# Performance work log

Hardware: AMD Instinct MI355X
Metric: run time of the kernel (lower is better)

## Reference

```python
import jax, jax.numpy as jnp
import numpy as np

B, S, D, UNITS = 8, 2048, 1024, 1024

def setup_inputs() -> dict:
    key = jax.random.key(0)
    k1, k2, k3, k4 = jax.random.split(key, 4)
    scale = 1.0 / np.sqrt(D)
    return {
        "inputs": jax.random.normal(k1, (B, S, D), dtype=jnp.float32),
        "Wq": jax.random.normal(k2, (D, UNITS), dtype=jnp.float32) * scale,
        "Wk": jax.random.normal(k3, (D, UNITS), dtype=jnp.float32) * scale,
        "Wv": jax.random.normal(k4, (D, UNITS), dtype=jnp.float32) * scale,
    }

def reference(inputs, Wq, Wk, Wv):
    # QKV projections (bias-free Dense): [B,S,D] @ [D,U] -> [B,S,U]
    q = jnp.einsum("bsd,du->bsu", inputs, Wq)
    k = jnp.einsum("bsd,du->bsu", inputs, Wk)
    v = jnp.einsum("bsd,du->bsu", inputs, Wv)
    # scaled dot-product scores [B,S,S]
    scores = jnp.einsum("bqu,bku->bqk", q, k) / jnp.sqrt(jnp.float32(UNITS))
    attn = jax.nn.softmax(scores, axis=-1)
    # weighted sum of values [B,S,U]
    return jnp.einsum("bqk,bku->bqu", attn, v)
```

## Files before the change

kernel.cpp:

```cpp
#include <hip/hip_runtime.h>


#define BM 128
#define BN 128
#define BK 64

typedef _Float16 half8  __attribute__((ext_vector_type(8)));
typedef _Float16 half4v __attribute__((ext_vector_type(4)));
typedef _Float16 half2v __attribute__((ext_vector_type(2)));
typedef float    floatx4 __attribute__((ext_vector_type(4)));

__device__ __forceinline__ void stage_async(const _Float16* __restrict__ src, int ld,
                                            _Float16* __restrict__ dst, int wave, int lane) {
#pragma unroll
    for (int i = 0; i < 4; ++i) {
        int chunk = i * 4 + wave;
        int L = chunk * 64 + lane;
        int row = L >> 3, c8 = L & 7;
        int cg = c8 ^ (row & 7);
        __builtin_amdgcn_global_load_lds(
            (const __attribute__((address_space(1))) unsigned int*)(src + (size_t)row * ld + cg * 8),
            (__attribute__((address_space(3))) unsigned int*)(dst + chunk * 512),
            16, 0, 0);
    }
}

__device__ __forceinline__ void mfma_accum(const _Float16* __restrict__ As,
                                           const _Float16* __restrict__ Bs,
                                           int wm, int wn, int l15, int q4,
                                           floatx4 acc[4][4]) {
#pragma unroll
    for (int kk = 0; kk < 2; ++kk) {
        half8 a[4], b[4];
#pragma unroll
        for (int i = 0; i < 4; ++i) {
            int row = wm * 64 + i * 16 + l15;
            int cg = (kk * 4 + q4) ^ (row & 7);
            a[i] = *(const half8*)(As + row * 64 + cg * 8);
        }
#pragma unroll
        for (int j = 0; j < 4; ++j) {
            int row = wn * 64 + j * 16 + l15;
            int cg = (kk * 4 + q4) ^ (row & 7);
            b[j] = *(const half8*)(Bs + row * 64 + cg * 8);
        }
#pragma unroll
        for (int i = 0; i < 4; ++i)
#pragma unroll
            for (int j = 0; j < 4; ++j)
                acc[i][j] = __builtin_amdgcn_mfma_f32_16x16x32_f16(a[i], b[j], acc[i][j], 0, 0, 0);
    }
}

__device__ __forceinline__ float sum8h(half8 a) {
    union { half8 v; half2v h2[4]; } u; u.v = a;
    half2v s0 = u.h2[0] + u.h2[1];
    half2v s1 = u.h2[2] + u.h2[3];
    half2v s  = s0 + s1;
    return (float)s[0] + (float)s[1];
}

__global__ void cast_x(const float* __restrict__ X, _Float16* __restrict__ Xh) {
    size_t i = ((size_t)blockIdx.x * 256 + threadIdx.x) * 8;
    float4 v0 = *(const float4*)(X + i);
    float4 v1 = *(const float4*)(X + i + 4);
    half8 hh;
    hh[0] = (_Float16)v0.x; hh[1] = (_Float16)v0.y; hh[2] = (_Float16)v0.z; hh[3] = (_Float16)v0.w;
    hh[4] = (_Float16)v1.x; hh[5] = (_Float16)v1.y; hh[6] = (_Float16)v1.z; hh[7] = (_Float16)v1.w;
    *(half8*)(Xh + i) = hh;
}

__global__ void prep_weights(const float* __restrict__ Wq, const float* __restrict__ Wk,
                             const float* __restrict__ Wv, _Float16* __restrict__ WbT) {
    int g = blockIdx.z;
    const float* W = (g == 0) ? Wq : (g == 1) ? Wk : Wv;
    __shared__ float tile[32][33];
    int u0 = blockIdx.x * 32, d0 = blockIdx.y * 32;
    int tx = threadIdx.x & 31, ty = threadIdx.x >> 5;
#pragma unroll
    for (int i = 0; i < 32; i += 8)
        tile[ty + i][tx] = W[(size_t)(d0 + ty + i) * 1024 + (u0 + tx)];
    __syncthreads();
#pragma unroll
    for (int i = 0; i < 32; i += 8)
        WbT[(size_t)g * 1024 * 1024 + (size_t)(u0 + ty + i) * 1024 + (d0 + tx)] =
            (_Float16)tile[tx][ty + i];
}

__global__ void qkv_gemm(const _Float16* __restrict__ Xh, const _Float16* __restrict__ WbT,
                         _Float16* __restrict__ Qh, _Float16* __restrict__ Kh,
                         _Float16* __restrict__ Vt) {
    __shared__ __align__(16) _Float16 As[BM * BK];
    __shared__ __align__(16) _Float16 Bs[BN * BK];
    int t = threadIdx.x;
    int lane = t & 63, wave = t >> 6;
    int wm = wave >> 1, wn = wave & 1;
    int l15 = lane & 15, q4 = lane >> 4;
    int m0 = blockIdx.y * BM, n0 = blockIdx.x * BN;
    floatx4 acc[4][4] = {};
    for (int kt = 0; kt < 1024; kt += BK) {
        __syncthreads();
        stage_async(Xh + (size_t)m0 * 1024 + kt, 1024, As, wave, lane);
        stage_async(WbT + (size_t)n0 * 1024 + kt, 1024, Bs, wave, lane);
        __syncthreads();
        mfma_accum(As, Bs, wm, wn, l15, q4, acc);
    }
    int which = blockIdx.x >> 3;
    int u0 = (blockIdx.x & 7) * BN;
    int b = m0 >> 11;
    int sbase = (m0 & 2047) + wm * 64;
    if (which < 2) {
        _Float16* dst = which ? Kh : Qh;
        _Float16* db = dst + (size_t)b * 2048 * 1024;
#pragma unroll
        for (int i = 0; i < 4; ++i)
#pragma unroll
            for (int j = 0; j < 4; ++j)
#pragma unroll
                for (int r = 0; r < 4; ++r) {
                    int s = sbase + i * 16 + q4 * 4 + r;
                    int u = u0 + wn * 64 + j * 16 + l15;
                    db[(size_t)s * 1024 + u] = (_Float16)acc[i][j][r];
                }
    } else {
        _Float16* vb = Vt + (size_t)b * 1024 * 2048;
#pragma unroll
        for (int i = 0; i < 4; ++i)
#pragma unroll
            for (int j = 0; j < 4; ++j) {
                int s = sbase + i * 16 + q4 * 4;
                int u = u0 + wn * 64 + j * 16 + l15;
                half4v pk;
#pragma unroll
                for (int r = 0; r < 4; ++r) pk[r] = (_Float16)acc[i][j][r];
                *(half4v*)(vb + (size_t)u * 2048 + s) = pk;
            }
    }
}

__global__ void scores_gemm(const _Float16* __restrict__ Qh, const _Float16* __restrict__ Kh,
                            _Float16* __restrict__ P) {
    __shared__ __align__(16) _Float16 As[BM * BK];
    __shared__ __align__(16) _Float16 Bs[BN * BK];
    int t = threadIdx.x;
    int lane = t & 63, wave = t >> 6;
    int wm = wave >> 1, wn = wave & 1;
    int l15 = lane & 15, q4 = lane >> 4;
    int m0 = blockIdx.y * BM, n0 = blockIdx.x * BN;
    int batch = blockIdx.z;
    const _Float16* A = Qh + (size_t)batch * 2048 * 1024;
    const _Float16* B = Kh + (size_t)batch * 2048 * 1024;
    floatx4 acc[4][4] = {};
    for (int kt = 0; kt < 1024; kt += BK) {
        __syncthreads();
        stage_async(A + (size_t)m0 * 1024 + kt, 1024, As, wave, lane);
        stage_async(B + (size_t)n0 * 1024 + kt, 1024, Bs, wave, lane);
        __syncthreads();
        mfma_accum(As, Bs, wm, wn, l15, q4, acc);
    }
    _Float16* Pb = P + (size_t)batch * 2048 * 2048;
#pragma unroll
    for (int i = 0; i < 4; ++i)
#pragma unroll
        for (int j = 0; j < 4; ++j)
#pragma unroll
            for (int r = 0; r < 4; ++r) {
                int m = m0 + wm * 64 + i * 16 + q4 * 4 + r;
                int n = n0 + wn * 64 + j * 16 + l15;
                Pb[(size_t)m * 2048 + n] = (_Float16)__expf(acc[i][j][r] * 0.03125f);
            }
}

__global__ void pv_gemm(const _Float16* __restrict__ P, const _Float16* __restrict__ Vt,
                        float* __restrict__ out) {
    __shared__ __align__(16) _Float16 As[BM * BK];
    __shared__ __align__(16) _Float16 Bs[BN * BK];
    int t = threadIdx.x;
    int lane = t & 63, wave = t >> 6;
    int wm = wave >> 1, wn = wave & 1;
    int l15 = lane & 15, q4 = lane >> 4;
    int m0 = blockIdx.y * BM, n0 = blockIdx.x * BN;
    int batch = blockIdx.z;
    const _Float16* A = P + (size_t)batch * 2048 * 2048;
    const _Float16* B = Vt + (size_t)batch * 1024 * 2048;
    floatx4 acc[4][4] = {};
    float rsum[4] = {0.f, 0.f, 0.f, 0.f};
    for (int kt = 0; kt < 2048; kt += BK) {
        __syncthreads();
        stage_async(A + (size_t)m0 * 2048 + kt, 2048, As, wave, lane);
        stage_async(B + (size_t)n0 * 2048 + kt, 2048, Bs, wave, lane);
        __syncthreads();
#pragma unroll
        for (int kk = 0; kk < 2; ++kk) {
            half8 a[4], b[4];
#pragma unroll
            for (int i = 0; i < 4; ++i) {
                int row = wm * 64 + i * 16 + l15;
                int cg = (kk * 4 + q4) ^ (row & 7);
                a[i] = *(const half8*)(As + row * 64 + cg * 8);
                rsum[i] += sum8h(a[i]);
            }
#pragma unroll
            for (int j = 0; j < 4; ++j) {
                int row = wn * 64 + j * 16 + l15;
                int cg = (kk * 4 + q4) ^ (row & 7);
                b[j] = *(const half8*)(Bs + row * 64 + cg * 8);
            }
#pragma unroll
            for (int i = 0; i < 4; ++i)
#pragma unroll
                for (int j = 0; j < 4; ++j)
                    acc[i][j] = __builtin_amdgcn_mfma_f32_16x16x32_f16(a[i], b[j], acc[i][j], 0, 0, 0);
        }
    }
    float rsumf[4];
#pragma unroll
    for (int i = 0; i < 4; ++i) {
        float v = rsum[i] + __shfl_xor(rsum[i], 16);
        rsumf[i] = v + __shfl_xor(v, 32);
    }
    float* ob = out + (size_t)batch * 2048 * 1024;
#pragma unroll
    for (int i = 0; i < 4; ++i)
#pragma unroll
        for (int r = 0; r < 4; ++r) {
            int rloc = q4 * 4 + r;
            float inv = 1.0f / __shfl(rsumf[i], rloc);
            int m = m0 + wm * 64 + i * 16 + rloc;
#pragma unroll
            for (int j = 0; j < 4; ++j) {
                int n = n0 + wn * 64 + j * 16 + l15;
                ob[(size_t)m * 1024 + n] = acc[i][j][r] * inv;
            }
        }
}

extern "C" void kernel_launch(void* const* d_in, const int* in_sizes, int n_in,
                              void* d_out, int out_size, void* d_ws, size_t ws_size,
                              hipStream_t stream) {
    const float* X  = (const float*)d_in[0];
    const float* Wq = (const float*)d_in[1];
    const float* Wk = (const float*)d_in[2];
    const float* Wv = (const float*)d_in[3];
    float* out = (float*)d_out;

    char* ws = (char*)d_ws;
    size_t off = 0;
    _Float16* Xh  = (_Float16*)(ws + off); off += (size_t)8 * 2048 * 1024 * 2;
    _Float16* WbT = (_Float16*)(ws + off); off += (size_t)3 * 1024 * 1024 * 2;
    _Float16* Qh  = (_Float16*)(ws + off); off += (size_t)8 * 2048 * 1024 * 2;
    _Float16* Kh  = (_Float16*)(ws + off); off += (size_t)8 * 2048 * 1024 * 2;
    _Float16* Vt  = (_Float16*)(ws + off); off += (size_t)8 * 1024 * 2048 * 2;
    _Float16* P   = (_Float16*)(ws + off); off += (size_t)8 * 2048 * 2048 * 2;

    cast_x      <<<dim3(8192, 1, 1), 256, 0, stream>>>(X, Xh);
    prep_weights<<<dim3(32, 32, 3), 256, 0, stream>>>(Wq, Wk, Wv, WbT);
    qkv_gemm    <<<dim3(24, 128, 1), 256, 0, stream>>>(Xh, WbT, Qh, Kh, Vt);
    scores_gemm <<<dim3(16, 16, 8),  256, 0, stream>>>(Qh, Kh, P);
    pv_gemm     <<<dim3(8, 16, 8),   256, 0, stream>>>(P, Vt, out);
}
```

Measured before the change: 398.6 us.

## Use 256x128 tiles with 8 waves for attention GEMMs and merge prep kernels

Scores and PV GEMMs now use 512-thread blocks covering 256x128 output tiles, halving the grid in M. Each block's staged K/V tile is reused across twice as many rows, which cuts global and LDS traffic per output. The X cast and weight transpose kernels are merged into one launch to save a kernel launch. The per-wave mapping (wm = wave>>1 over 4 rows of 64) appears to cover 256 rows with 8 waves, and the larger blocks raise LDS use per block and may reduce the number of resident blocks.

```diff
diff --git a/kernel.cpp b/kernel.cpp
--- a/kernel.cpp
+++ b/kernel.cpp
@@ -1,8 +1,6 @@
 #include <hip/hip_runtime.h>
 
 
-#define BM 128
-#define BN 128
 #define BK 64
 
 typedef _Float16 half8  __attribute__((ext_vector_type(8)));
@@ -10,11 +8,12 @@
 typedef _Float16 half2v __attribute__((ext_vector_type(2)));
 typedef float    floatx4 __attribute__((ext_vector_type(4)));
 
+template <int ITERS, int NWAVES>
 __device__ __forceinline__ void stage_async(const _Float16* __restrict__ src, int ld,
                                             _Float16* __restrict__ dst, int wave, int lane) {
 #pragma unroll
-    for (int i = 0; i < 4; ++i) {
-        int chunk = i * 4 + wave;
+    for (int i = 0; i < ITERS; ++i) {
+        int chunk = i * NWAVES + wave;
         int L = chunk * 64 + lane;
         int row = L >> 3, c8 = L & 7;
         int cg = c8 ^ (row & 7);
@@ -60,58 +59,60 @@
     return (float)s[0] + (float)s[1];
 }
 
-__global__ void cast_x(const float* __restrict__ X, _Float16* __restrict__ Xh) {
-    size_t i = ((size_t)blockIdx.x * 256 + threadIdx.x) * 8;
-    float4 v0 = *(const float4*)(X + i);
-    float4 v1 = *(const float4*)(X + i + 4);
-    half8 hh;
-    hh[0] = (_Float16)v0.x; hh[1] = (_Float16)v0.y; hh[2] = (_Float16)v0.z; hh[3] = (_Float16)v0.w;
-    hh[4] = (_Float16)v1.x; hh[5] = (_Float16)v1.y; hh[6] = (_Float16)v1.z; hh[7] = (_Float16)v1.w;
-    *(half8*)(Xh + i) = hh;
-}
-
-__global__ void prep_weights(const float* __restrict__ Wq, const float* __restrict__ Wk,
-                             const float* __restrict__ Wv, _Float16* __restrict__ WbT) {
-    int g = blockIdx.z;
-    const float* W = (g == 0) ? Wq : (g == 1) ? Wk : Wv;
-    __shared__ float tile[32][33];
-    int u0 = blockIdx.x * 32, d0 = blockIdx.y * 32;
-    int tx = threadIdx.x & 31, ty = threadIdx.x >> 5;
-#pragma unroll
-    for (int i = 0; i < 32; i += 8)
-        tile[ty + i][tx] = W[(size_t)(d0 + ty + i) * 1024 + (u0 + tx)];
-    __syncthreads();
-#pragma unroll
-    for (int i = 0; i < 32; i += 8)
-        WbT[(size_t)g * 1024 * 1024 + (size_t)(u0 + ty + i) * 1024 + (d0 + tx)] =
-            (_Float16)tile[tx][ty + i];
+__global__ void prep_all(const float* __restrict__ X, const float* __restrict__ Wq,
+                         const float* __restrict__ Wk, const float* __restrict__ Wv,
+                         _Float16* __restrict__ Xh, _Float16* __restrict__ WbT) {
+    int bx = blockIdx.x;
+    if (bx < 8192) {
+        size_t i = ((size_t)bx * 256 + threadIdx.x) * 8;
+        float4 v0 = *(const float4*)(X + i);
+        float4 v1 = *(const float4*)(X + i + 4);
+        half8 hh;
+        hh[0] = (_Float16)v0.x; hh[1] = (_Float16)v0.y; hh[2] = (_Float16)v0.z; hh[3] = (_Float16)v0.w;
+        hh[4] = (_Float16)v1.x; hh[5] = (_Float16)v1.y; hh[6] = (_Float16)v1.z; hh[7] = (_Float16)v1.w;
+        *(half8*)(Xh + i) = hh;
+    } else {
+        int wb = bx - 8192;
+        int g = wb >> 10, rem = wb & 1023;
+        const float* W = (g == 0) ? Wq : (g == 1) ? Wk : Wv;
+        __shared__ float tile[32][33];
+        int u0 = (rem & 31) * 32, d0 = (rem >> 5) * 32;
+        int tx = threadIdx.x & 31, ty = threadIdx.x >> 5;
+#pragma unroll
+        for (int i = 0; i < 32; i += 8)
+            tile[ty + i][tx] = W[(size_t)(d0 + ty + i) * 1024 + (u0 + tx)];
+        __syncthreads();
+#pragma unroll
+        for (int i = 0; i < 32; i += 8)
+            WbT[(size_t)g * 1024 * 1024 + (size_t)(u0 + ty + i) * 1024 + (d0 + tx)] =
+                (_Float16)tile[tx][ty + i];
+    }
 }
 
 __global__ void qkv_gemm(const _Float16* __restrict__ Xh, const _Float16* __restrict__ WbT,
                          _Float16* __restrict__ Qh, _Float16* __restrict__ Kh,
                          _Float16* __restrict__ Vt) {
-    __shared__ __align__(16) _Float16 As[BM * BK];
-    __shared__ __align__(16) _Float16 Bs[BN * BK];
+    __shared__ __align__(16) _Float16 As[128 * BK];
+    __shared__ __align__(16) _Float16 Bs[128 * BK];
     int t = threadIdx.x;
     int lane = t & 63, wave = t >> 6;
     int wm = wave >> 1, wn = wave & 1;
     int l15 = lane & 15, q4 = lane >> 4;
-    int m0 = blockIdx.y * BM, n0 = blockIdx.x * BN;
+    int m0 = blockIdx.y * 128, n0 = blockIdx.x * 128;
     floatx4 acc[4][4] = {};
     for (int kt = 0; kt < 1024; kt += BK) {
         __syncthreads();
-        stage_async(Xh + (size_t)m0 * 1024 + kt, 1024, As, wave, lane);
-        stage_async(WbT + (size_t)n0 * 1024 + kt, 1024, Bs, wave, lane);
+        stage_async<4, 4>(Xh + (size_t)m0 * 1024 + kt, 1024, As, wave, lane);
+        stage_async<4, 4>(WbT + (size_t)n0 * 1024 + kt, 1024, Bs, wave, lane);
         __syncthreads();
         mfma_accum(As, Bs, wm, wn, l15, q4, acc);
     }
     int which = blockIdx.x >> 3;
-    int u0 = (blockIdx.x & 7) * BN;
+    int u0 = (blockIdx.x & 7) * 128;
     int b = m0 >> 11;
     int sbase = (m0 & 2047) + wm * 64;
     if (which < 2) {
-        _Float16* dst = which ? Kh : Qh;
-        _Float16* db = dst + (size_t)b * 2048 * 1024;
+        _Float16* db = (which ? Kh : Qh) + (size_t)b * 2048 * 1024;
 #pragma unroll
         for (int i = 0; i < 4; ++i)
 #pragma unroll
@@ -138,23 +139,24 @@
     }
 }
 
-__global__ void scores_gemm(const _Float16* __restrict__ Qh, const _Float16* __restrict__ Kh,
-                            _Float16* __restrict__ P) {
-    __shared__ __align__(16) _Float16 As[BM * BK];
-    __shared__ __align__(16) _Float16 Bs[BN * BK];
+__global__ void __launch_bounds__(512)
+scores_gemm(const _Float16* __restrict__ Qh, const _Float16* __restrict__ Kh,
+            _Float16* __restrict__ P) {
+    __shared__ __align__(16) _Float16 As[256 * BK];
+    __shared__ __align__(16) _Float16 Bs[128 * BK];
     int t = threadIdx.x;
     int lane = t & 63, wave = t >> 6;
     int wm = wave >> 1, wn = wave & 1;
     int l15 = lane & 15, q4 = lane >> 4;
-    int m0 = blockIdx.y * BM, n0 = blockIdx.x * BN;
+    int m0 = blockIdx.y * 256, n0 = blockIdx.x * 128;
     int batch = blockIdx.z;
     const _Float16* A = Qh + (size_t)batch * 2048 * 1024;
     const _Float16* B = Kh + (size_t)batch * 2048 * 1024;
     floatx4 acc[4][4] = {};
     for (int kt = 0; kt < 1024; kt += BK) {
         __syncthreads();
-        stage_async(A + (size_t)m0 * 1024 + kt, 1024, As, wave, lane);
-        stage_async(B + (size_t)n0 * 1024 + kt, 1024, Bs, wave, lane);
+        stage_async<4, 8>(A + (size_t)m0 * 1024 + kt, 1024, As, wave, lane);
+        stage_async<2, 8>(B + (size_t)n0 * 1024 + kt, 1024, Bs, wave, lane);
         __syncthreads();
         mfma_accum(As, Bs, wm, wn, l15, q4, acc);
     }
@@ -171,15 +173,16 @@
             }
 }
 
-__global__ void pv_gemm(const _Float16* __restrict__ P, const _Float16* __restrict__ Vt,
-                        float* __restrict__ out) {
-    __shared__ __align__(16) _Float16 As[BM * BK];
-    __shared__ __align__(16) _Float16 Bs[BN * BK];
+__global__ void __launch_bounds__(512)
+pv_gemm(const _Float16* __restrict__ P, const _Float16* __restrict__ Vt,
+        float* __restrict__ out) {
+    __shared__ __align__(16) _Float16 As[256 * BK];
+    __shared__ __align__(16) _Float16 Bs[128 * BK];
     int t = threadIdx.x;
     int lane = t & 63, wave = t >> 6;
     int wm = wave >> 1, wn = wave & 1;
     int l15 = lane & 15, q4 = lane >> 4;
-    int m0 = blockIdx.y * BM, n0 = blockIdx.x * BN;
+    int m0 = blockIdx.y * 256, n0 = blockIdx.x * 128;
     int batch = blockIdx.z;
     const _Float16* A = P + (size_t)batch * 2048 * 2048;
     const _Float16* B = Vt + (size_t)batch * 1024 * 2048;
@@ -187,8 +190,8 @@
     float rsum[4] = {0.f, 0.f, 0.f, 0.f};
     for (int kt = 0; kt < 2048; kt += BK) {
         __syncthreads();
-        stage_async(A + (size_t)m0 * 2048 + kt, 2048, As, wave, lane);
-        stage_async(B + (size_t)n0 * 2048 + kt, 2048, Bs, wave, lane);
+        stage_async<4, 8>(A + (size_t)m0 * 2048 + kt, 2048, As, wave, lane);
+        stage_async<2, 8>(B + (size_t)n0 * 2048 + kt, 2048, Bs, wave, lane);
         __syncthreads();
 #pragma unroll
         for (int kk = 0; kk < 2; ++kk) {
@@ -253,9 +256,8 @@
     _Float16* Vt  = (_Float16*)(ws + off); off += (size_t)8 * 1024 * 2048 * 2;
     _Float16* P   = (_Float16*)(ws + off); off += (size_t)8 * 2048 * 2048 * 2;
 
-    cast_x      <<<dim3(8192, 1, 1), 256, 0, stream>>>(X, Xh);
-    prep_weights<<<dim3(32, 32, 3), 256, 0, stream>>>(Wq, Wk, Wv, WbT);
-    qkv_gemm    <<<dim3(24, 128, 1), 256, 0, stream>>>(Xh, WbT, Qh, Kh, Vt);
-    scores_gemm <<<dim3(16, 16, 8),  256, 0, stream>>>(Qh, Kh, P);
-    pv_gemm     <<<dim3(8, 16, 8),   256, 0, stream>>>(P, Vt, out);
-}
+    prep_all   <<<dim3(11264, 1, 1), 256, 0, stream>>>(X, Wq, Wk, Wv, Xh, WbT);
+    qkv_gemm   <<<dim3(24, 128, 1), 256, 0, stream>>>(Xh, WbT, Qh, Kh, Vt);
+    scores_gemm<<<dim3(16, 8, 8),  512, 0, stream>>>(Qh, Kh, P);
+    pv_gemm    <<<dim3(8, 8, 8),   512, 0, stream>>>(P, Vt, out);
+}
```

Measured after the change: 414.6 us. +4.0%, slower.
